# Performance work log

Measured on AMD Instinct MI355X. Metric: run time of the kernel, lower is better.

The kernel has to match this reference:

```python
import jax, jax.numpy as jnp
import numpy as np

B, S, D = 4, 2048, 1024
NEG_BIG = -1.0e9


def setup_inputs() -> dict:
    key = jax.random.key(0)
    ks = jax.random.split(key, 9)
    scale = 1.0 / np.sqrt(D)
    inp = {
        "v": jax.random.normal(ks[0], (B, S, D), dtype=jnp.float32),
        "k": jax.random.normal(ks[1], (B, S, D), dtype=jnp.float32),
        "q": jax.random.normal(ks[2], (B, S, D), dtype=jnp.float32),
        # causal mask: 1 where attention is disallowed (j > i), broadcast over batch
        "mask": jnp.triu(jnp.ones((1, S, S), dtype=jnp.float32), k=1),
        "Wq": jax.random.normal(ks[3], (D, D), dtype=jnp.float32) * scale,
        "bq": jnp.zeros((D,), dtype=jnp.float32),
        "Wk": jax.random.normal(ks[4], (D, D), dtype=jnp.float32) * scale,
        "bk": jnp.zeros((D,), dtype=jnp.float32),
        "Wv": jax.random.normal(ks[5], (D, D), dtype=jnp.float32) * scale,
        "bv": jnp.zeros((D,), dtype=jnp.float32),
    }
    return inp


def reference(v, k, q, mask, Wq, bq, Wk, bk, Wv, bv):
    # Dense projections (Keras Dense: x @ W + b)
    qp = q @ Wq + bq  # [B, S, D]
    kp = k @ Wk + bk  # [B, S, D]
    vp = v @ Wv + bv  # [B, S, D]

    dk = jnp.asarray(D, dtype=qp.dtype)
    logits = jnp.einsum("bqd,bkd->bqk", qp, kp) / jnp.sqrt(dk)  # [B, S, S]
    logits = logits + mask * NEG_BIG
    attn = jax.nn.softmax(logits, axis=-1)  # [B, S, S]
    out = jnp.einsum("bqk,bkd->bqd", attn, vp)  # [B, S, D]
    return out, attn
```

## Files before the change

kernel.cpp:

```cpp
#include <hip/hip_runtime.h>
#include <hip/hip_bf16.h>
#include <cstdint>

#define BATCH 4
#define S_LEN 2048
#define D_DIM 1024

typedef __attribute__((ext_vector_type(4))) float f32x4_t;
typedef __attribute__((ext_vector_type(8))) __bf16 bf16x8_t;

__device__ __forceinline__ ushort f32_to_bf16(float f) {
    uint32_t u = __float_as_uint(f);
    uint32_t r = (u + 0x7FFFu + ((u >> 16) & 1u)) >> 16;
    return (ushort)r;
}

__global__ __launch_bounds__(256)
void cvt3_kernel(const float* __restrict__ a, const float* __restrict__ b,
                 const float* __restrict__ c, ushort* __restrict__ out, int n4) {
    int z = blockIdx.y;
    const float* src = (z == 0) ? a : ((z == 1) ? b : c);
    ushort* dst = out + (size_t)z * n4 * 4;
    int idx = blockIdx.x * blockDim.x + threadIdx.x;
    int stride = gridDim.x * blockDim.x;
    const float4* in4 = (const float4*)src;
    ushort4* out4 = (ushort4*)dst;
    for (int i = idx; i < n4; i += stride) {
        float4 v = in4[i];
        ushort4 o;
        o.x = f32_to_bf16(v.x);
        o.y = f32_to_bf16(v.y);
        o.z = f32_to_bf16(v.z);
        o.w = f32_to_bf16(v.w);
        out4[i] = o;
    }
}

__global__ __launch_bounds__(256)
void transpose_cvt_kernel(const float* __restrict__ in, ushort* __restrict__ out,
                          int rows, int cols) {
    __shared__ ushort tile[64][66];
    int r0 = blockIdx.y * 64, c0 = blockIdx.x * 64;
    int t = threadIdx.x;
    int cr = t & 63;
    int cc = t >> 6;
    #pragma unroll
    for (int i = 0; i < 16; ++i) {
        int r = cc * 16 + i;
        tile[r][cr] = f32_to_bf16(in[(size_t)(r0 + r) * cols + (c0 + cr)]);
    }
    __syncthreads();
    #pragma unroll
    for (int i = 0; i < 16; ++i) {
        int c = cc * 16 + i;
        out[(size_t)(c0 + c) * rows + (r0 + cr)] = tile[cr][c];
    }
}

__global__ __launch_bounds__(256)
void transpose_bf16_kernel(const ushort* __restrict__ in, ushort* __restrict__ out,
                           int rows, int cols, int lda, long strideA, long strideB) {
    __shared__ ushort tile[64][66];
    const ushort* src = in + (size_t)blockIdx.z * strideA;
    ushort* dst = out + (size_t)blockIdx.z * strideB;
    int r0 = blockIdx.y * 64, c0 = blockIdx.x * 64;
    int t = threadIdx.x;
    int cr = t & 63;
    int cc = t >> 6;
    #pragma unroll
    for (int i = 0; i < 16; ++i) {
        int r = cc * 16 + i;
        tile[r][cr] = src[(size_t)(r0 + r) * lda + (c0 + cr)];
    }
    __syncthreads();
    #pragma unroll
    for (int i = 0; i < 16; ++i) {
        int c = cc * 16 + i;
        dst[(size_t)(c0 + c) * rows + (r0 + cr)] = tile[cr][c];
    }
}

__global__ __launch_bounds__(256)
void bias_concat_kernel(const float* __restrict__ bq, const float* __restrict__ bk,
                        const float* __restrict__ bv, float* __restrict__ out) {
    int i = blockIdx.x * blockDim.x + threadIdx.x;
    if (i < D_DIM) out[i] = bq[i];
    else if (i < 2 * D_DIM) out[i] = bk[i - D_DIM];
    else if (i < 3 * D_DIM) out[i] = bv[i - 2 * D_DIM];
}

enum { MODE_PROJ = 0, MODE_LOGITS = 1, MODE_OUT = 2 };

#define LGKM(N) do { asm volatile("s_waitcnt lgkmcnt(" #N ")" ::: "memory"); \
    __builtin_amdgcn_sched_barrier(0); } while (0)
#define GATE(N) do { asm volatile("s_waitcnt vmcnt(" #N ")" ::: "memory"); \
    __builtin_amdgcn_sched_barrier(0); } while (0)

#define GLOAD(dst, src) __builtin_amdgcn_global_load_lds( \
    (const __attribute__((address_space(1))) uint32_t*)(src), \
    (__attribute__((address_space(3))) uint32_t*)(dst), 16, 0, 0)

__device__ __forceinline__ void xcd_swizzle(int& bc, int& br) {
    int gx = gridDim.x;
    int nwg = gx * gridDim.y;
    int orig = blockIdx.y * gx + blockIdx.x;
    int xcd = orig & 7, idx = orig >> 3;
    int wgid = xcd * (nwg >> 3) + idx;
    bc = wgid % gx;
    br = wgid / gx;
}

template<int MODE>
__global__ __launch_bounds__(512, 2)
void gemm_pipe_kernel(const ushort* __restrict__ A, const ushort* __restrict__ Bt,
                      const float* __restrict__ bias, void* __restrict__ Cout,
                      int K, int lda, int ldb, int ldc,
                      long strideA, long strideB, long strideC, float scale) {
    __shared__ ushort As[3][256 * 64];
    __shared__ ushort Bs[3][128 * 64];
    int bc, br;
    xcd_swizzle(bc, br);
    int bz = blockIdx.z;
    if (MODE == MODE_LOGITS && bc > 2 * br + 1) return;
    const ushort* Ab = (MODE == MODE_PROJ) ? A + (size_t)(bc >> 3) * strideA
                                           : A + (size_t)bz * strideA;
    const ushort* Bb = Bt + (size_t)bz * strideB;
    int brow = br * 256, bcol = bc * 128;
    int t = threadIdx.x, lane = t & 63, wid = t >> 6;
    int wr = wid >> 1, wc = wid & 1;
    int nkt = K / 64;
    if (MODE == MODE_OUT) nkt = min(nkt, (brow + 256) / 64);

    const ushort* aSrc[4];
    const ushort* bSrc[2];
    int oA[4], oB[2];
    #pragma unroll
    for (int j = 0; j < 4; ++j) {
        int o = (j * 512 + t) * 16;
        int row = o >> 7;
        int col = (o & 127) ^ ((row & 7) << 4);
        oA[j] = o >> 1;
        aSrc[j] = Ab + (size_t)(brow + row) * lda + (col >> 1);
    }
    #pragma unroll
    for (int j = 0; j < 2; ++j) {
        int o = (j * 512 + t) * 16;
        int row = o >> 7;
        int col = (o & 127) ^ ((row & 7) << 4);
        oB[j] = o >> 1;
        bSrc[j] = Bb + (size_t)(bcol + row) * ldb + (col >> 1);
    }
    auto stage = [&](int tk, int slot) {
        ushort* dA = &As[slot][0];
        ushort* dB = &Bs[slot][0];
        #pragma unroll
        for (int j = 0; j < 4; ++j) GLOAD(dA + oA[j], aSrc[j] + tk * 64);
        #pragma unroll
        for (int j = 0; j < 2; ++j) GLOAD(dB + oB[j], bSrc[j] + tk * 64);
    };

    int rdA[4][2], rdB[4][2];
    #pragma unroll
    for (int m = 0; m < 4; ++m) {
        int ra = wr * 64 + m * 16 + (lane & 15);
        #pragma unroll
        for (int ks = 0; ks < 2; ++ks) {
            int cb = ks * 64 + ((lane >> 4) * 16);
            rdA[m][ks] = ra * 128 + (cb ^ ((ra & 7) << 4));
        }
    }
    #pragma unroll
    for (int n = 0; n < 4; ++n) {
        int rb = wc * 64 + n * 16 + (lane & 15);
        #pragma unroll
        for (int ks = 0; ks < 2; ++ks) {
            int cb = ks * 64 + ((lane >> 4) * 16);
            rdB[n][ks] = rb * 128 + (cb ^ ((rb & 7) << 4));
        }
    }

    f32x4_t acc[4][4];
    #pragma unroll
    for (int m = 0; m < 4; ++m)
        #pragma unroll
        for (int n = 0; n < 4; ++n)
            acc[m][n] = (f32x4_t){0.f, 0.f, 0.f, 0.f};

    bf16x8_t aE0[4], aE1[4], bE0[4], bE1[4];
    bf16x8_t aO0[4], aO1[4], bO0[4], bO1[4];

#define MF16(AV, BV)                                                           \
    do { __builtin_amdgcn_s_setprio(1);                                        \
        _Pragma("unroll") for (int m = 0; m < 4; ++m)                          \
        _Pragma("unroll") for (int n = 0; n < 4; ++n)                          \
            acc[m][n] = __builtin_amdgcn_mfma_f32_16x16x32_bf16(               \
                AV[m], BV[n], acc[m][n], 0, 0, 0);                             \
        __builtin_amdgcn_s_setprio(0); } while (0)

#define TILE_BODY(X, CA0, CA1, CB0, CB1, NA0, NA1, NB0, NB1)                   \
    do {                                                                       \
        int x_ = (X);                                                          \
        __builtin_amdgcn_s_barrier();             \
        if (x_ + 2 < nkt) stage(x_ + 2, (x_ + 2) % 3);                         \
        if (x_ + 1 < nkt) { if (x_ + 2 < nkt) { GATE(6); } else { GATE(0); } } \
        __builtin_amdgcn_s_barrier();             \
        {                                                                      \
            const char* nA = (const char*)&As[(x_ + 1) % 3][0];                \
            const char* nB = (const char*)&Bs[(x_ + 1) % 3][0];                \
            if (x_ + 1 < nkt) {                                                \
                _Pragma("unroll") for (int n = 0; n < 4; ++n)                  \
                    NB0[n] = *(const bf16x8_t*)(nB + rdB[n][0]);               \
                _Pragma("unroll") for (int m = 0; m < 4; ++m)                  \
                    NA0[m] = *(const bf16x8_t*)(nA + rdA[m][0]);               \
                LGKM(8);                  \
            } else { LGKM(0); }                                                \
            MF16(CA0, CB0);                                                    \
            if (x_ + 1 < nkt) {                                                \
                _Pragma("unroll") for (int n = 0; n < 4; ++n)                  \
                    NB1[n] = *(const bf16x8_t*)(nB + rdB[n][1]);               \
                _Pragma("unroll") for (int m = 0; m < 4; ++m)                  \
                    NA1[m] = *(const bf16x8_t*)(nA + rdA[m][1]);               \
            }                                                                  \
            MF16(CA1, CB1);                                                    \
        }                                                                      \
    } while (0)

    stage(0, 0);
    stage(1, 1);
    GATE(6);
    __builtin_amdgcn_s_barrier();
    {
        const char* pA = (const char*)&As[0][0];
        const char* pB = (const char*)&Bs[0][0];
        #pragma unroll
        for (int n = 0; n < 4; ++n) bE0[n] = *(const bf16x8_t*)(pB + rdB[n][0]);
        #pragma unroll
        for (int m = 0; m < 4; ++m) aE0[m] = *(const bf16x8_t*)(pA + rdA[m][0]);
        #pragma unroll
        for (int n = 0; n < 4; ++n) bE1[n] = *(const bf16x8_t*)(pB + rdB[n][1]);
        #pragma unroll
        for (int m = 0; m < 4; ++m) aE1[m] = *(const bf16x8_t*)(pA + rdA[m][1]);
    }

    int nhalf = nkt >> 1;
    for (int it = 0; it < nhalf; ++it) {
        int x = 2 * it;
        TILE_BODY(x,     aE0, aE1, bE0, bE1, aO0, aO1, bO0, bO1);
        TILE_BODY(x + 1, aO0, aO1, bO0, bO1, aE0, aE1, bE0, bE1);
    }
#undef TILE_BODY
#undef MF16

    int crow0 = brow + wr * 64 + ((lane >> 4) * 4);
    int ccol0 = bcol + wc * 64 + (lane & 15);
    if (MODE == MODE_PROJ) {
        ushort* C = (ushort*)Cout;
        #pragma unroll
        for (int mf = 0; mf < 4; ++mf) {
            #pragma unroll
            for (int nf = 0; nf < 4; ++nf) {
                int col = ccol0 + nf * 16;
                float bv = bias[col];
                #pragma unroll
                for (int j = 0; j < 4; ++j) {
                    int rowg = crow0 + mf * 16 + j;
                    C[(size_t)rowg * ldc + col] = f32_to_bf16(acc[mf][nf][j] + bv);
                }
            }
        }
    } else {
        float* C = (float*)Cout + (size_t)bz * strideC;
        #pragma unroll
        for (int mf = 0; mf < 4; ++mf)
            #pragma unroll
            for (int nf = 0; nf < 4; ++nf) {
                int col = ccol0 + nf * 16;
                #pragma unroll
                for (int j = 0; j < 4; ++j) {
                    int rowg = crow0 + mf * 16 + j;
                    C[(size_t)rowg * ldc + col] = acc[mf][nf][j] * scale;
                }
            }
    }
}

__global__ __launch_bounds__(256)
void softmax_causal_kernel(float* __restrict__ attn, ushort* __restrict__ attn_bf) {
    int rowid = blockIdx.x;
    int i = rowid & (S_LEN - 1);
    float* lrow = attn + (size_t)rowid * S_LEN;
    ushort* brw = attn_bf + (size_t)rowid * S_LEN;
    int t = threadIdx.x;
    int nvalid = i + 1;

    float vals[8];
    float lmax = -1e30f;
    #pragma unroll
    for (int it = 0; it < 8; ++it) {
        int j = it * 256 + t;
        float v = (j < nvalid) ? lrow[j] : -1e30f;
        vals[it] = v;
        lmax = fmaxf(lmax, v);
    }
    #pragma unroll
    for (int off = 32; off > 0; off >>= 1)
        lmax = fmaxf(lmax, __shfl_xor(lmax, off));

    __shared__ float redm[4];
    __shared__ float reds[4];
    int wave = t >> 6, lane = t & 63;
    if (lane == 0) redm[wave] = lmax;
    __syncthreads();
    float m = fmaxf(fmaxf(redm[0], redm[1]), fmaxf(redm[2], redm[3]));

    float lsum = 0.f;
    #pragma unroll
    for (int it = 0; it < 8; ++it) {
        int j = it * 256 + t;
        float e = (j < nvalid) ? __expf(vals[it] - m) : 0.f;
        vals[it] = e;
        lsum += e;
    }
    #pragma unroll
    for (int off = 32; off > 0; off >>= 1)
        lsum += __shfl_xor(lsum, off);
    if (lane == 0) reds[wave] = lsum;
    __syncthreads();
    float denom = reds[0] + reds[1] + reds[2] + reds[3];
    float inv = 1.f / denom;

    #pragma unroll
    for (int it = 0; it < 8; ++it) {
        int j = it * 256 + t;
        float p = vals[it] * inv;
        lrow[j] = p;
        brw[j] = f32_to_bf16(p);
    }
}

extern "C" void kernel_launch(void* const* d_in, const int* in_sizes, int n_in,
                              void* d_out, int out_size, void* d_ws, size_t ws_size,
                              hipStream_t stream) {
    const float* v  = (const float*)d_in[0];
    const float* k  = (const float*)d_in[1];
    const float* q  = (const float*)d_in[2];
    const float* Wq = (const float*)d_in[4];
    const float* bq = (const float*)d_in[5];
    const float* Wk = (const float*)d_in[6];
    const float* bk = (const float*)d_in[7];
    const float* Wv = (const float*)d_in[8];
    const float* bv = (const float*)d_in[9];

    float* out  = (float*)d_out;
    float* attn = (float*)d_out + (size_t)BATCH * S_LEN * D_DIM;

    char* ws = (char*)d_ws;
    const size_t NTOK = (size_t)BATCH * S_LEN;
    const size_t XSZ  = NTOK * D_DIM * sizeof(ushort);
    ushort* xqkv  = (ushort*)(ws);
    ushort* qkvp  = (ushort*)(ws + 3 * XSZ);
    ushort* WT    = (ushort*)(ws + 6 * XSZ);
    float*  bias3 = (float*)(ws + 6 * XSZ + 3 * (size_t)D_DIM * D_DIM * sizeof(ushort));
    ushort* vpT     = (ushort*)(ws);
    ushort* attn_bf = (ushort*)(ws + XSZ);

    const int n4 = (int)(NTOK * D_DIM / 4);
    cvt3_kernel<<<dim3(1024, 3), dim3(256), 0, stream>>>(q, k, v, xqkv, n4);

    transpose_cvt_kernel<<<dim3(16, 16), dim3(256), 0, stream>>>(Wq, WT, D_DIM, D_DIM);
    transpose_cvt_kernel<<<dim3(16, 16), dim3(256), 0, stream>>>(Wk, WT + (size_t)D_DIM * D_DIM, D_DIM, D_DIM);
    transpose_cvt_kernel<<<dim3(16, 16), dim3(256), 0, stream>>>(Wv, WT + 2 * (size_t)D_DIM * D_DIM, D_DIM, D_DIM);
    bias_concat_kernel<<<dim3(12), dim3(256), 0, stream>>>(bq, bk, bv, bias3);

    gemm_pipe_kernel<MODE_PROJ><<<dim3(24, 32, 1), dim3(512), 0, stream>>>(
        xqkv, WT, bias3, qkvp, D_DIM, D_DIM, D_DIM, 3 * D_DIM,
        (long)NTOK * D_DIM, 0, 0, 1.f);

    transpose_bf16_kernel<<<dim3(D_DIM / 64, S_LEN / 64, BATCH), dim3(256), 0, stream>>>(
        qkvp + 2 * D_DIM, vpT, S_LEN, D_DIM, 3 * D_DIM,
        (long)S_LEN * 3 * D_DIM, (long)D_DIM * S_LEN);

    gemm_pipe_kernel<MODE_LOGITS><<<dim3(16, 8, BATCH), dim3(512), 0, stream>>>(
        qkvp, qkvp + D_DIM, nullptr, attn, D_DIM, 3 * D_DIM, 3 * D_DIM, S_LEN,
        (long)S_LEN * 3 * D_DIM, (long)S_LEN * 3 * D_DIM, (long)S_LEN * S_LEN, 0.03125f);

    softmax_causal_kernel<<<dim3((int)NTOK), dim3(256), 0, stream>>>(attn, attn_bf);

    gemm_pipe_kernel<MODE_OUT><<<dim3(8, 8, BATCH), dim3(512), 0, stream>>>(
        attn_bf, vpT, nullptr, out, S_LEN, S_LEN, S_LEN, D_DIM,
        (long)S_LEN * S_LEN, (long)D_DIM * S_LEN, (long)S_LEN * D_DIM, 1.f);
}
```

Measured before the change: 241.6 us.

## Use 256x256 ping-pong GEMM for projection/logits, fuse V transpose into epilogue

Adds a new GEMM kernel with 256x256 tiles, double-buffered LDS and a four-quadrant MFMA schedule separated by barriers. It is used for the QKV projection and the causal logits, where tiles above the diagonal are skipped. The projection epilogue now writes V transposed straight into vpT, which removes the separate transpose kernel. The softmax skips the fully masked 256-column chunks and writes zeros there instead. The larger tiles raise register and LDS pressure, and the transposed V stores are strided, which may hurt write coalescing.

After: 220.0 us. -8.9%, faster.

```diff
diff --git a/kernel.cpp b/kernel.cpp
--- a/kernel.cpp
+++ b/kernel.cpp
@@ -58,29 +58,6 @@
 }
 
 __global__ __launch_bounds__(256)
-void transpose_bf16_kernel(const ushort* __restrict__ in, ushort* __restrict__ out,
-                           int rows, int cols, int lda, long strideA, long strideB) {
-    __shared__ ushort tile[64][66];
-    const ushort* src = in + (size_t)blockIdx.z * strideA;
-    ushort* dst = out + (size_t)blockIdx.z * strideB;
-    int r0 = blockIdx.y * 64, c0 = blockIdx.x * 64;
-    int t = threadIdx.x;
-    int cr = t & 63;
-    int cc = t >> 6;
-    #pragma unroll
-    for (int i = 0; i < 16; ++i) {
-        int r = cc * 16 + i;
-        tile[r][cr] = src[(size_t)(r0 + r) * lda + (c0 + cr)];
-    }
-    __syncthreads();
-    #pragma unroll
-    for (int i = 0; i < 16; ++i) {
-        int c = cc * 16 + i;
-        dst[(size_t)(c0 + c) * rows + (r0 + cr)] = tile[cr][c];
-    }
-}
-
-__global__ __launch_bounds__(256)
 void bias_concat_kernel(const float* __restrict__ bq, const float* __restrict__ bk,
                         const float* __restrict__ bv, float* __restrict__ out) {
     int i = blockIdx.x * blockDim.x + threadIdx.x;
@@ -91,8 +68,11 @@
 
 enum { MODE_PROJ = 0, MODE_LOGITS = 1, MODE_OUT = 2 };
 
-#define LGKM(N) do { asm volatile("s_waitcnt lgkmcnt(" #N ")" ::: "memory"); \
+#define PRE_BAR() do { __builtin_amdgcn_s_barrier(); \
+    asm volatile("s_waitcnt lgkmcnt(0)" ::: "memory"); \
     __builtin_amdgcn_sched_barrier(0); } while (0)
+#define POST_BAR() do { __builtin_amdgcn_sched_barrier(0); \
+    __builtin_amdgcn_s_barrier(); } while (0)
 #define GATE(N) do { asm volatile("s_waitcnt vmcnt(" #N ")" ::: "memory"); \
     __builtin_amdgcn_sched_barrier(0); } while (0)
 
@@ -112,24 +92,189 @@
 
 template<int MODE>
 __global__ __launch_bounds__(512, 2)
-void gemm_pipe_kernel(const ushort* __restrict__ A, const ushort* __restrict__ Bt,
-                      const float* __restrict__ bias, void* __restrict__ Cout,
-                      int K, int lda, int ldb, int ldc,
-                      long strideA, long strideB, long strideC, float scale) {
+void gemm_q_kernel(const ushort* __restrict__ A, const ushort* __restrict__ Bt,
+                   const float* __restrict__ bias, void* __restrict__ Cout,
+                   ushort* __restrict__ vpT,
+                   int K, int lda, int ldb, int ldc,
+                   long strideA, long strideC, float scale) {
+    __shared__ ushort As[2][256 * 64];
+    __shared__ ushort Bs[2][256 * 64];
+    int bc, br;
+    xcd_swizzle(bc, br);
+    int bz = blockIdx.z;
+    if (MODE == MODE_LOGITS && bc > br) return;
+    const ushort* Ab = (MODE == MODE_PROJ) ? A + (size_t)(bc >> 2) * strideA
+                                           : A + (size_t)bz * strideA;
+    const ushort* Bb = (MODE == MODE_PROJ) ? Bt : Bt + (size_t)bz * strideA;
+    int brow = br * 256, bcol = bc * 256;
+    int t = threadIdx.x, lane = t & 63, wid = t >> 6;
+    int wr = wid >> 2, wc = wid & 3;
+    int nkt = K / 64;
+
+    const ushort* aSrc[4];
+    const ushort* bSrc[4];
+    int oL[4];
+    #pragma unroll
+    for (int j = 0; j < 4; ++j) {
+        int o = (j * 512 + t) * 16;
+        int row = o >> 7;
+        int colb = (o & 127) ^ ((row & 7) << 4);
+        oL[j] = o >> 1;
+        aSrc[j] = Ab + (size_t)(brow + row) * lda + (colb >> 1);
+        bSrc[j] = Bb + (size_t)(bcol + row) * ldb + (colb >> 1);
+    }
+    auto stgA = [&](int tk, int slot, int j0, int j1) {
+        ushort* d = &As[slot][0];
+        GLOAD(d + oL[j0], aSrc[j0] + tk * 64);
+        GLOAD(d + oL[j1], aSrc[j1] + tk * 64);
+    };
+    auto stgB = [&](int tk, int slot, int j0, int j1) {
+        ushort* d = &Bs[slot][0];
+        GLOAD(d + oL[j0], bSrc[j0] + tk * 64);
+        GLOAD(d + oL[j1], bSrc[j1] + tk * 64);
+    };
+
+    int rdA[2][4], rdB[4];
+    #pragma unroll
+    for (int mh = 0; mh < 2; ++mh)
+        #pragma unroll
+        for (int m = 0; m < 4; ++m) {
+            int ra = wr * 128 + mh * 64 + m * 16 + (lane & 15);
+            int cb = (lane >> 4) * 16;
+            rdA[mh][m] = ra * 128 + (cb ^ ((ra & 7) << 4));
+        }
+    #pragma unroll
+    for (int nf = 0; nf < 4; ++nf) {
+        int rb = (nf >> 1) * 128 + wc * 32 + (nf & 1) * 16 + (lane & 15);
+        int cb = (lane >> 4) * 16;
+        rdB[nf] = rb * 128 + (cb ^ ((rb & 7) << 4));
+    }
+
+    f32x4_t acc[8][4];
+    #pragma unroll
+    for (int m = 0; m < 8; ++m)
+        #pragma unroll
+        for (int n = 0; n < 4; ++n)
+            acc[m][n] = (f32x4_t){0.f, 0.f, 0.f, 0.f};
+
+    bf16x8_t af[4][2], bfr[4][2];
+
+    auto readAh = [&](int slot, int mh) {
+        const char* base = (const char*)&As[slot][0];
+        #pragma unroll
+        for (int m = 0; m < 4; ++m) {
+            af[m][0] = *(const bf16x8_t*)(base + rdA[mh][m]);
+            af[m][1] = *(const bf16x8_t*)(base + (rdA[mh][m] ^ 64));
+        }
+    };
+    auto readBh = [&](int slot, int nh) {
+        const char* base = (const char*)&Bs[slot][0];
+        #pragma unroll
+        for (int n = 0; n < 2; ++n) {
+            int nf = nh * 2 + n;
+            bfr[nf][0] = *(const bf16x8_t*)(base + rdB[nf]);
+            bfr[nf][1] = *(const bf16x8_t*)(base + (rdB[nf] ^ 64));
+        }
+    };
+
+#define QUAD(MH, NH)                                                                \
+    do { __builtin_amdgcn_s_setprio(1);                                             \
+        _Pragma("unroll") for (int m = 0; m < 4; ++m)                               \
+        _Pragma("unroll") for (int n = 0; n < 2; ++n)                               \
+        _Pragma("unroll") for (int ks = 0; ks < 2; ++ks)                            \
+            acc[(MH) * 4 + m][(NH) * 2 + n] = __builtin_amdgcn_mfma_f32_16x16x32_bf16( \
+                af[m][ks], bfr[(NH) * 2 + n][ks], acc[(MH) * 4 + m][(NH) * 2 + n], 0, 0, 0); \
+        __builtin_amdgcn_s_setprio(0); } while (0)
+
+    stgB(0, 0, 0, 1); stgA(0, 0, 0, 2); stgB(0, 0, 2, 3); stgA(0, 0, 1, 3);
+    GATE(4);
+    __builtin_amdgcn_s_barrier();
+
+    for (int y = 0; y < nkt; ++y) {
+        int cur = y & 1, nxt = cur ^ 1;
+        bool st = (y + 1 < nkt);
+        readAh(cur, 0); readBh(cur, 0);
+        if (st) stgB(y + 1, nxt, 0, 1);
+        PRE_BAR(); QUAD(0, 0);
+        if (st) { GATE(4); } else { GATE(2); }
+        POST_BAR();
+        readBh(cur, 1);
+        if (st) stgA(y + 1, nxt, 0, 2);
+        PRE_BAR(); QUAD(0, 1);
+        if (st) { GATE(4); } else { GATE(0); }
+        POST_BAR();
+        readAh(cur, 1);
+        if (st) stgB(y + 1, nxt, 2, 3);
+        PRE_BAR(); QUAD(1, 1); POST_BAR();
+        if (st) stgA(y + 1, nxt, 1, 3);
+        PRE_BAR(); QUAD(1, 0);
+        if (st) { GATE(4); }
+        POST_BAR();
+    }
+#undef QUAD
+
+    int crow0 = brow + wr * 128 + ((lane >> 4) * 4);
+    int ccol0 = wc * 32 + (lane & 15);
+    if (MODE == MODE_PROJ) {
+        #pragma unroll
+        for (int mf = 0; mf < 8; ++mf) {
+            int rowg = crow0 + (mf >> 2) * 64 + (mf & 3) * 16;
+            #pragma unroll
+            for (int nf = 0; nf < 4; ++nf) {
+                int gcol = bcol + (nf >> 1) * 128 + ccol0 + (nf & 1) * 16;
+                float bv = bias[gcol];
+                if (bc < 8) {
+                    ushort* C = (ushort*)Cout;
+                    #pragma unroll
+                    for (int j = 0; j < 4; ++j)
+                        C[(size_t)(rowg + j) * 2048 + gcol] = f32_to_bf16(acc[mf][nf][j] + bv);
+                } else {
+                    int d = gcol - 2048;
+                    int b = rowg >> 11, s = rowg & 2047;
+                    ushort4 o;
+                    o.x = f32_to_bf16(acc[mf][nf][0] + bv);
+                    o.y = f32_to_bf16(acc[mf][nf][1] + bv);
+                    o.z = f32_to_bf16(acc[mf][nf][2] + bv);
+                    o.w = f32_to_bf16(acc[mf][nf][3] + bv);
+                    *(ushort4*)&vpT[(size_t)b * D_DIM * S_LEN + (size_t)d * S_LEN + s] = o;
+                }
+            }
+        }
+    } else {
+        float* C = (float*)Cout + (size_t)bz * strideC;
+        #pragma unroll
+        for (int mf = 0; mf < 8; ++mf) {
+            int rowg = crow0 + (mf >> 2) * 64 + (mf & 3) * 16;
+            #pragma unroll
+            for (int nf = 0; nf < 4; ++nf) {
+                int col = bcol + (nf >> 1) * 128 + ccol0 + (nf & 1) * 16;
+                #pragma unroll
+                for (int j = 0; j < 4; ++j)
+                    C[(size_t)(rowg + j) * ldc + col] = acc[mf][nf][j] * scale;
+            }
+        }
+    }
+}
+
+#define LGKM(N) do { asm volatile("s_waitcnt lgkmcnt(" #N ")" ::: "memory"); \
+    __builtin_amdgcn_sched_barrier(0); } while (0)
+
+__global__ __launch_bounds__(512, 2)
+void gemm_out_kernel(const ushort* __restrict__ A, const ushort* __restrict__ Bt,
+                     void* __restrict__ Cout,
+                     int K, int lda, int ldb, int ldc,
+                     long strideA, long strideB, long strideC, float scale) {
     __shared__ ushort As[3][256 * 64];
     __shared__ ushort Bs[3][128 * 64];
     int bc, br;
     xcd_swizzle(bc, br);
     int bz = blockIdx.z;
-    if (MODE == MODE_LOGITS && bc > 2 * br + 1) return;
-    const ushort* Ab = (MODE == MODE_PROJ) ? A + (size_t)(bc >> 3) * strideA
-                                           : A + (size_t)bz * strideA;
+    const ushort* Ab = A + (size_t)bz * strideA;
     const ushort* Bb = Bt + (size_t)bz * strideB;
     int brow = br * 256, bcol = bc * 128;
     int t = threadIdx.x, lane = t & 63, wid = t >> 6;
     int wr = wid >> 1, wc = wid & 1;
-    int nkt = K / 64;
-    if (MODE == MODE_OUT) nkt = min(nkt, (brow + 256) / 64);
+    int nkt = min(K / 64, (brow + 256) / 64);
 
     const ushort* aSrc[4];
     const ushort* bSrc[2];
@@ -200,10 +345,10 @@
 #define TILE_BODY(X, CA0, CA1, CB0, CB1, NA0, NA1, NB0, NB1)                   \
     do {                                                                       \
         int x_ = (X);                                                          \
-        __builtin_amdgcn_s_barrier();             \
+        __builtin_amdgcn_s_barrier();                                          \
         if (x_ + 2 < nkt) stage(x_ + 2, (x_ + 2) % 3);                         \
         if (x_ + 1 < nkt) { if (x_ + 2 < nkt) { GATE(6); } else { GATE(0); } } \
-        __builtin_amdgcn_s_barrier();             \
+        __builtin_amdgcn_s_barrier();                                          \
         {                                                                      \
             const char* nA = (const char*)&As[(x_ + 1) % 3][0];                \
             const char* nB = (const char*)&Bs[(x_ + 1) % 3][0];                \
@@ -212,7 +357,7 @@
                     NB0[n] = *(const bf16x8_t*)(nB + rdB[n][0]);               \
                 _Pragma("unroll") for (int m = 0; m < 4; ++m)                  \
                     NA0[m] = *(const bf16x8_t*)(nA + rdA[m][0]);               \
-                LGKM(8);                  \
+                LGKM(8);                                                       \
             } else { LGKM(0); }                                                \
             MF16(CA0, CB0);                                                    \
             if (x_ + 1 < nkt) {                                                \
@@ -251,37 +396,20 @@
 #undef TILE_BODY
 #undef MF16
 
+    float* C = (float*)Cout + (size_t)bz * strideC;
     int crow0 = brow + wr * 64 + ((lane >> 4) * 4);
     int ccol0 = bcol + wc * 64 + (lane & 15);
-    if (MODE == MODE_PROJ) {
-        ushort* C = (ushort*)Cout;
-        #pragma unroll
-        for (int mf = 0; mf < 4; ++mf) {
+    #pragma unroll
+    for (int mf = 0; mf < 4; ++mf)
+        #pragma unroll
+        for (int nf = 0; nf < 4; ++nf) {
+            int col = ccol0 + nf * 16;
             #pragma unroll
-            for (int nf = 0; nf < 4; ++nf) {
-                int col = ccol0 + nf * 16;
-                float bv = bias[col];
-                #pragma unroll
-                for (int j = 0; j < 4; ++j) {
-                    int rowg = crow0 + mf * 16 + j;
-                    C[(size_t)rowg * ldc + col] = f32_to_bf16(acc[mf][nf][j] + bv);
-                }
+            for (int j = 0; j < 4; ++j) {
+                int rowg = crow0 + mf * 16 + j;
+                C[(size_t)rowg * ldc + col] = acc[mf][nf][j] * scale;
             }
         }
-    } else {
-        float* C = (float*)Cout + (size_t)bz * strideC;
-        #pragma unroll
-        for (int mf = 0; mf < 4; ++mf)
-            #pragma unroll
-            for (int nf = 0; nf < 4; ++nf) {
-                int col = ccol0 + nf * 16;
-                #pragma unroll
-                for (int j = 0; j < 4; ++j) {
-                    int rowg = crow0 + mf * 16 + j;
-                    C[(size_t)rowg * ldc + col] = acc[mf][nf][j] * scale;
-                }
-            }
-    }
 }
 
 __global__ __launch_bounds__(256)
@@ -292,15 +420,18 @@
     ushort* brw = attn_bf + (size_t)rowid * S_LEN;
     int t = threadIdx.x;
     int nvalid = i + 1;
+    int nact = (nvalid + 255) >> 8;
 
     float vals[8];
     float lmax = -1e30f;
     #pragma unroll
     for (int it = 0; it < 8; ++it) {
-        int j = it * 256 + t;
-        float v = (j < nvalid) ? lrow[j] : -1e30f;
-        vals[it] = v;
-        lmax = fmaxf(lmax, v);
+        if (it < nact) {
+            int j = it * 256 + t;
+            float v = (j < nvalid) ? lrow[j] : -1e30f;
+            vals[it] = v;
+            lmax = fmaxf(lmax, v);
+        }
     }
     #pragma unroll
     for (int off = 32; off > 0; off >>= 1)
@@ -316,10 +447,12 @@
     float lsum = 0.f;
     #pragma unroll
     for (int it = 0; it < 8; ++it) {
-        int j = it * 256 + t;
-        float e = (j < nvalid) ? __expf(vals[it] - m) : 0.f;
-        vals[it] = e;
-        lsum += e;
+        if (it < nact) {
+            int j = it * 256 + t;
+            float e = (j < nvalid) ? __expf(vals[it] - m) : 0.f;
+            vals[it] = e;
+            lsum += e;
+        }
     }
     #pragma unroll
     for (int off = 32; off > 0; off >>= 1)
@@ -332,9 +465,14 @@
     #pragma unroll
     for (int it = 0; it < 8; ++it) {
         int j = it * 256 + t;
-        float p = vals[it] * inv;
-        lrow[j] = p;
-        brw[j] = f32_to_bf16(p);
+        if (it < nact) {
+            float p = vals[it] * inv;
+            lrow[j] = p;
+            brw[j] = f32_to_bf16(p);
+        } else {
+            lrow[j] = 0.f;
+            brw[j] = 0;
+        }
     }
 }
 
@@ -356,13 +494,12 @@
 
     char* ws = (char*)d_ws;
     const size_t NTOK = (size_t)BATCH * S_LEN;
-    const size_t XSZ  = NTOK * D_DIM * sizeof(ushort);
     ushort* xqkv  = (ushort*)(ws);
-    ushort* qkvp  = (ushort*)(ws + 3 * XSZ);
-    ushort* WT    = (ushort*)(ws + 6 * XSZ);
-    float*  bias3 = (float*)(ws + 6 * XSZ + 3 * (size_t)D_DIM * D_DIM * sizeof(ushort));
-    ushort* vpT     = (ushort*)(ws);
-    ushort* attn_bf = (ushort*)(ws + XSZ);
+    ushort* qkvp  = (ushort*)(ws + 48u * 1024 * 1024);
+    ushort* vpT   = (ushort*)(ws + 80u * 1024 * 1024);
+    ushort* WT    = (ushort*)(ws + 96u * 1024 * 1024);
+    float*  bias3 = (float*)(ws + 102u * 1024 * 1024);
+    ushort* attn_bf = (ushort*)(ws);
 
     const int n4 = (int)(NTOK * D_DIM / 4);
     cvt3_kernel<<<dim3(1024, 3), dim3(256), 0, stream>>>(q, k, v, xqkv, n4);
@@ -372,21 +509,17 @@
     transpose_cvt_kernel<<<dim3(16, 16), dim3(256), 0, stream>>>(Wv, WT + 2 * (size_t)D_DIM * D_DIM, D_DIM, D_DIM);
     bias_concat_kernel<<<dim3(12), dim3(256), 0, stream>>>(bq, bk, bv, bias3);
 
-    gemm_pipe_kernel<MODE_PROJ><<<dim3(24, 32, 1), dim3(512), 0, stream>>>(
-        xqkv, WT, bias3, qkvp, D_DIM, D_DIM, D_DIM, 3 * D_DIM,
-        (long)NTOK * D_DIM, 0, 0, 1.f);
-
-    transpose_bf16_kernel<<<dim3(D_DIM / 64, S_LEN / 64, BATCH), dim3(256), 0, stream>>>(
-        qkvp + 2 * D_DIM, vpT, S_LEN, D_DIM, 3 * D_DIM,
-        (long)S_LEN * 3 * D_DIM, (long)D_DIM * S_LEN);
-
-    gemm_pipe_kernel<MODE_LOGITS><<<dim3(16, 8, BATCH), dim3(512), 0, stream>>>(
-        qkvp, qkvp + D_DIM, nullptr, attn, D_DIM, 3 * D_DIM, 3 * D_DIM, S_LEN,
-        (long)S_LEN * 3 * D_DIM, (long)S_LEN * 3 * D_DIM, (long)S_LEN * S_LEN, 0.03125f);
+    gemm_q_kernel<MODE_PROJ><<<dim3(12, 32, 1), dim3(512), 0, stream>>>(
+        xqkv, WT, bias3, qkvp, vpT, D_DIM, D_DIM, D_DIM, 2048,
+        (long)NTOK * D_DIM, 0, 1.f);
+
+    gemm_q_kernel<MODE_LOGITS><<<dim3(8, 8, BATCH), dim3(512), 0, stream>>>(
+        qkvp, qkvp + D_DIM, nullptr, attn, nullptr, D_DIM, 2048, 2048, S_LEN,
+        (long)S_LEN * 2048, (long)S_LEN * S_LEN, 0.03125f);
 
     softmax_causal_kernel<<<dim3((int)NTOK), dim3(256), 0, stream>>>(attn, attn_bf);
 
-    gemm_pipe_kernel<MODE_OUT><<<dim3(8, 8, BATCH), dim3(512), 0, stream>>>(
-        attn_bf, vpT, nullptr, out, S_LEN, S_LEN, S_LEN, D_DIM,
+    gemm_out_kernel<<<dim3(8, 8, BATCH), dim3(512), 0, stream>>>(
+        attn_bf, vpT, out, S_LEN, S_LEN, S_LEN, D_DIM,
         (long)S_LEN * S_LEN, (long)D_DIM * S_LEN, (long)S_LEN * D_DIM, 1.f);
 }
```
